# Kernel tuning notes

Hardware: AMD Instinct MI355X
Metric: run time of the kernel (lower is better)

## Reference

```python
import jax, jax.numpy as jnp
import numpy as np

BN_EPS = 1e-3  # Keras BatchNormalization default epsilon

def _conv2d_same(x, w, b):
    # x: NHWC, w: HWIO (kh,kw,2,1)
    y = jax.lax.conv_general_dilated(x, w, window_strides=(1, 1), padding='SAME',
                                     dimension_numbers=('NHWC', 'HWIO', 'NHWC'))
    return y + b

def _zpool(t):
    # concat([max, avg], axis=-1) over channel axis -> last dim = 2
    return jnp.concatenate([jnp.max(t, axis=-1, keepdims=True),
                            jnp.mean(t, axis=-1, keepdims=True)], axis=-1)

def _att_map(t2, w, b, g, beta, mean, var):
    y = _conv2d_same(t2, w, b)
    y = (y - mean) * jax.lax.rsqrt(var + BN_EPS) * g + beta  # inference BN
    return jax.nn.sigmoid(y)

def setup_inputs() -> dict:
    key = jax.random.key(0)
    ks = jax.random.split(key, 8)
    B, H, W, C, K, RR = 32, 56, 56, 256, 7, 8
    d = {}
    d['x'] = jax.random.normal(ks[0], (B, H, W, C), dtype=jnp.float32)
    for i, kk in zip((1, 2, 3), ks[1:4]):
        d[f'conv{i}_w'] = jax.random.normal(kk, (K, K, 2, 1), dtype=jnp.float32) * 0.1
        d[f'conv{i}_b'] = jnp.zeros((1,), dtype=jnp.float32)
        d[f'bn{i}_g'] = jnp.ones((1,), dtype=jnp.float32)
        d[f'bn{i}_b'] = jnp.zeros((1,), dtype=jnp.float32)
        d[f'bn{i}_m'] = jnp.zeros((1,), dtype=jnp.float32)
        d[f'bn{i}_v'] = jnp.ones((1,), dtype=jnp.float32)
    Ch = C // RR
    d['se_w1'] = jax.random.normal(ks[4], (C, Ch), dtype=jnp.float32) * (2.0 / C) ** 0.5
    d['se_b1'] = jnp.zeros((Ch,), dtype=jnp.float32)
    d['se_w2'] = jax.random.normal(ks[5], (Ch, C), dtype=jnp.float32) * 0.05
    d['se_b2'] = jnp.zeros((C,), dtype=jnp.float32)
    return d

def reference(x, conv1_w, conv1_b, bn1_g, bn1_b, bn1_m, bn1_v,
              conv2_w, conv2_b, bn2_g, bn2_b, bn2_m, bn2_v,
              conv3_w, conv3_b, bn3_g, bn3_b, bn3_m, bn3_v,
              se_w1, se_b1, se_w2, se_b2):
    # Branch 1 (H-axis): permute (B,H,W,C)->(B,H,C,W), pool over W
    th1 = jnp.transpose(x, (0, 1, 3, 2))
    a1 = _att_map(_zpool(th1), conv1_w, conv1_b, bn1_g, bn1_b, bn1_m, bn1_v)
    br1 = jnp.transpose(th1 * a1, (0, 1, 3, 2))
    # Branch 2 (W-axis): permute (B,H,W,C)->(B,C,W,H), pool over H
    th2 = jnp.transpose(x, (0, 3, 2, 1))
    a2 = _att_map(_zpool(th2), conv2_w, conv2_b, bn2_g, bn2_b, bn2_m, bn2_v)
    br2 = jnp.transpose(th2 * a2, (0, 3, 2, 1))
    # Branch 3 (identity): pool over C
    a3 = _att_map(_zpool(x), conv3_w, conv3_b, bn3_g, bn3_b, bn3_m, bn3_v)
    br3 = x * a3
    # TriSE1: Add branches, then SE channel gating
    s = br1 + br2 + br3
    gap = jnp.mean(s, axis=(1, 2), keepdims=True)            # (B,1,1,C)
    h = jax.nn.relu(jnp.einsum('bijc,cd->bijd', gap, se_w1) + se_b1)
    cw = jax.nn.sigmoid(jnp.einsum('bijd,dc->bijc', h, se_w2) + se_b2)
    return s * cw
```

## Files before the change

kernel.cpp:

```cpp
#include <hip/hip_runtime.h>
#include <math.h>

namespace {
constexpr int B = 32, H = 56, W = 56, C = 256;
constexpr int HW  = H * W;
constexpr int WC  = W * C;
constexpr int HC  = H * C;
constexpr int HWC = H * W * C;
constexpr int CH  = 32;
constexpr float BN_EPS = 1e-3f;

using f4v = __attribute__((ext_vector_type(4))) float;

__device__ __forceinline__ float sigmoidf_(float v) { return 1.0f / (1.0f + expf(-v)); }

__device__ __forceinline__ void nt_store_float4(float* p, const float4& o) {
    union { float4 s; f4v v; } u;
    u.s = o;
    __builtin_nontemporal_store(u.v, (f4v*)p);
}
}

__global__ __launch_bounds__(256)
void pool_all_kernel(const float* __restrict__ x,
                     float* __restrict__ pmax1, float* __restrict__ pavg1,
                     float* __restrict__ pmax2, float* __restrict__ pavg2,
                     float* __restrict__ pmax3, float* __restrict__ pavg3) {
    const int t = threadIdx.x;
    const int lane = t & 63, sub = t >> 6;
    const int c4 = lane * 4;
    __shared__ float smx[4][256];
    __shared__ float ssm[4][256];

    if (blockIdx.x < B * H) {
        const int b = blockIdx.x / H, h = blockIdx.x % H;
        const float* xp = x + (size_t)b * HWC + (size_t)h * WC + c4;
        float4 v[14];
        #pragma unroll
        for (int wq = 0; wq < 14; ++wq)
            v[wq] = *(const float4*)(xp + (wq * 4 + sub) * C);
        float4 mx = v[0], sm = v[0];
        #pragma unroll
        for (int wq = 1; wq < 14; ++wq) {
            mx.x = fmaxf(mx.x, v[wq].x); mx.y = fmaxf(mx.y, v[wq].y);
            mx.z = fmaxf(mx.z, v[wq].z); mx.w = fmaxf(mx.w, v[wq].w);
            sm.x += v[wq].x; sm.y += v[wq].y; sm.z += v[wq].z; sm.w += v[wq].w;
        }
        #pragma unroll
        for (int wq = 0; wq < 14; ++wq) {
            float m3 = fmaxf(fmaxf(v[wq].x, v[wq].y), fmaxf(v[wq].z, v[wq].w));
            float s3 = v[wq].x + v[wq].y + v[wq].z + v[wq].w;
            #pragma unroll
            for (int off = 32; off > 0; off >>= 1) {
                m3 = fmaxf(m3, __shfl_down(m3, off));
                s3 += __shfl_down(s3, off);
            }
            if (lane == 0) {
                const int w = wq * 4 + sub;
                pmax3[b * HW + h * W + w] = m3;
                pavg3[b * HW + h * W + w] = s3 * (1.0f / C);
            }
        }
        *(float4*)&smx[sub][c4] = mx;
        *(float4*)&ssm[sub][c4] = sm;
        __syncthreads();
        const float m = fmaxf(fmaxf(smx[0][t], smx[1][t]), fmaxf(smx[2][t], smx[3][t]));
        const float s = ssm[0][t] + ssm[1][t] + ssm[2][t] + ssm[3][t];
        pmax1[b * HC + h * C + t] = m;
        pavg1[b * HC + h * C + t] = s * (1.0f / W);
    } else {
        const int tt = blockIdx.x - B * H;
        const int b = tt / W, w = tt % W;
        const float* xp = x + (size_t)b * HWC + (size_t)w * C + c4;
        float4 v[14];
        #pragma unroll
        for (int i = 0; i < 14; ++i)
            v[i] = *(const float4*)(xp + (size_t)(i * 4 + sub) * WC);
        float4 mx = v[0], sm = v[0];
        #pragma unroll
        for (int i = 1; i < 14; ++i) {
            mx.x = fmaxf(mx.x, v[i].x); mx.y = fmaxf(mx.y, v[i].y);
            mx.z = fmaxf(mx.z, v[i].z); mx.w = fmaxf(mx.w, v[i].w);
            sm.x += v[i].x; sm.y += v[i].y; sm.z += v[i].z; sm.w += v[i].w;
        }
        *(float4*)&smx[sub][c4] = mx;
        *(float4*)&ssm[sub][c4] = sm;
        __syncthreads();
        const float m = fmaxf(fmaxf(smx[0][t], smx[1][t]), fmaxf(smx[2][t], smx[3][t]));
        const float s = ssm[0][t] + ssm[1][t] + ssm[2][t] + ssm[3][t];
        pmax2[(size_t)b * WC + w * C + t] = m;
        pavg2[(size_t)b * WC + w * C + t] = s * (1.0f / H);
    }
}

__global__ __launch_bounds__(256)
void conv_all_kernel(const float* __restrict__ pmax1, const float* __restrict__ pavg1,
                     const float* __restrict__ pmax2, const float* __restrict__ pavg2,
                     const float* __restrict__ pmax3, const float* __restrict__ pavg3,
                     const float* __restrict__ c1w, const float* __restrict__ c1b,
                     const float* __restrict__ g1,  const float* __restrict__ be1,
                     const float* __restrict__ m1,  const float* __restrict__ v1,
                     const float* __restrict__ c2w, const float* __restrict__ c2b,
                     const float* __restrict__ g2,  const float* __restrict__ be2,
                     const float* __restrict__ m2,  const float* __restrict__ v2,
                     const float* __restrict__ c3w, const float* __restrict__ c3b,
                     const float* __restrict__ g3,  const float* __restrict__ be3,
                     const float* __restrict__ m3,  const float* __restrict__ v3,
                     float* __restrict__ a1, float* __restrict__ a2t, float* __restrict__ a3) {
    const int t = threadIdx.x;
    __shared__ float wg[98];
    __shared__ float2 sp[7][264];

    if (blockIdx.x < B * H) {
        if (t < 98) wg[t] = c1w[t];
        const int b = blockIdx.x / H, h = blockIdx.x % H;
        const float* bm = pmax1 + (size_t)b * HC;
        const float* ba = pavg1 + (size_t)b * HC;
        #pragma unroll
        for (int ky = 0; ky < 7; ++ky) {
            const int hy = h + ky - 3;
            const bool val = (hy >= 0 && hy < H);
            const int hyc = min(max(hy, 0), H - 1);
            const float lm = bm[hyc * C + t];
            const float la = ba[hyc * C + t];
            sp[ky][t + 3] = val ? make_float2(lm, la) : make_float2(0.f, 0.f);
            if (t < 3) { sp[ky][t] = make_float2(0.f, 0.f); sp[ky][261 - t] = make_float2(0.f, 0.f); }
        }
        __syncthreads();
        const float A  = rsqrtf(v1[0] + BN_EPS) * g1[0];
        const float Bc = (c1b[0] - m1[0]) * A + be1[0];
        float acc = 0.f;
        #pragma unroll
        for (int ky = 0; ky < 7; ++ky)
            #pragma unroll
            for (int kx = 0; kx < 7; ++kx) {
                const float2 p = sp[ky][t + kx];
                acc += p.x * wg[ky * 14 + kx * 2] + p.y * wg[ky * 14 + kx * 2 + 1];
            }
        a1[b * HC + h * C + t] = sigmoidf_(acc * A + Bc);
    } else if (blockIdx.x < 2 * B * H) {
        if (t < 98) wg[t] = c2w[t];
        const int tt = blockIdx.x - B * H;
        const int b = tt / W, w = tt % W;
        #pragma unroll
        for (int kx = 0; kx < 7; ++kx) {
            const int wx = w + kx - 3;
            const bool val = (wx >= 0 && wx < W);
            const int wxc = min(max(wx, 0), W - 1);
            const float lm = pmax2[(size_t)b * WC + wxc * C + t];
            const float la = pavg2[(size_t)b * WC + wxc * C + t];
            sp[kx][t + 3] = val ? make_float2(lm, la) : make_float2(0.f, 0.f);
            if (t < 3) { sp[kx][t] = make_float2(0.f, 0.f); sp[kx][261 - t] = make_float2(0.f, 0.f); }
        }
        __syncthreads();
        const float A  = rsqrtf(v2[0] + BN_EPS) * g2[0];
        const float Bc = (c2b[0] - m2[0]) * A + be2[0];
        float acc = 0.f;
        #pragma unroll
        for (int kx = 0; kx < 7; ++kx)
            #pragma unroll
            for (int ky = 0; ky < 7; ++ky) {
                const float2 p = sp[kx][t + ky];
                acc += p.x * wg[ky * 14 + kx * 2] + p.y * wg[ky * 14 + kx * 2 + 1];
            }
        a2t[(size_t)b * WC + w * C + t] = sigmoidf_(acc * A + Bc);
    } else {
        if (t < 98) wg[t] = c3w[t];
        float2 (*sp3)[66] = (float2(*)[66])sp;
        const int tt = blockIdx.x - 2 * B * H;
        const int b = tt / 14, h0 = (tt % 14) * 4;
        const float* bm = pmax3 + (size_t)b * HW;
        const float* ba = pavg3 + (size_t)b * HW;
        for (int idx = t; idx < 10 * 62; idx += 256) {
            const int r = idx / 62, col = idx % 62;
            const int hh = h0 + r - 3, ww = col - 3;
            const bool val = (hh >= 0 && hh < H && ww >= 0 && ww < W);
            const int hs = min(max(hh, 0), H - 1), wsx = min(max(ww, 0), W - 1);
            const float pm = bm[hs * W + wsx];
            const float pa = ba[hs * W + wsx];
            sp3[r][col] = val ? make_float2(pm, pa) : make_float2(0.f, 0.f);
        }
        __syncthreads();
        if (t < 224) {
            const int r = t / 56, w = t % 56;
            const float A  = rsqrtf(v3[0] + BN_EPS) * g3[0];
            const float Bc = (c3b[0] - m3[0]) * A + be3[0];
            float acc = 0.f;
            #pragma unroll
            for (int ky = 0; ky < 7; ++ky)
                #pragma unroll
                for (int kx = 0; kx < 7; ++kx) {
                    const float2 p = sp3[r + ky][w + kx];
                    acc += p.x * wg[ky * 14 + kx * 2] + p.y * wg[ky * 14 + kx * 2 + 1];
                }
            a3[b * HW + (h0 + r) * W + w] = sigmoidf_(acc * A + Bc);
        }
    }
}

__global__ __launch_bounds__(256)
void gap_row_kernel(const float* __restrict__ x, const float* __restrict__ a3,
                    float* __restrict__ gpart) {
    const int b = blockIdx.x / H, h = blockIdx.x % H;
    const int t = threadIdx.x;
    const int lane = t & 63, sub = t >> 6;
    const int c4 = lane * 4;
    const float* xp = x + (size_t)b * HWC + (size_t)h * WC + c4;
    const float* ap = a3 + b * HW + h * W + sub;
    float4 v[14]; float av[14];
    #pragma unroll
    for (int wq = 0; wq < 14; ++wq) {
        v[wq]  = *(const float4*)(xp + (wq * 4 + sub) * C);
        av[wq] = ap[wq * 4];
    }
    float4 acc = make_float4(0.f, 0.f, 0.f, 0.f);
    #pragma unroll
    for (int wq = 0; wq < 14; ++wq) {
        acc.x += v[wq].x * av[wq];
        acc.y += v[wq].y * av[wq];
        acc.z += v[wq].z * av[wq];
        acc.w += v[wq].w * av[wq];
    }
    __shared__ float sacc[4][256];
    *(float4*)&sacc[sub][c4] = acc;
    __syncthreads();
    gpart[(size_t)blockIdx.x * C + t] = sacc[0][t] + sacc[1][t] + sacc[2][t] + sacc[3][t];
}

__global__ __launch_bounds__(256)
void se_kernel(const float* __restrict__ gpart,
               const float* __restrict__ a1,  const float* __restrict__ pavg1,
               const float* __restrict__ a2t, const float* __restrict__ pavg2,
               const float* __restrict__ w1, const float* __restrict__ b1,
               const float* __restrict__ w2, const float* __restrict__ b2,
               float* __restrict__ cw) {
    const int b = blockIdx.x;
    const int t = threadIdx.x;
    __shared__ float gs[C];
    __shared__ float part[8][33];
    __shared__ float hs[CH];
    const float* pa = a1    + (size_t)b * HC + t;
    const float* pv = pavg1 + (size_t)b * HC + t;
    const float* qa = a2t   + (size_t)b * WC + t;
    const float* qv = pavg2 + (size_t)b * WC + t;
    const float* gp = gpart + (size_t)b * H * C + t;
    float s1 = 0.f, s2 = 0.f, s3 = 0.f;
    #pragma unroll 8
    for (int r = 0; r < H; ++r) {
        s1 += pa[r * C] * pv[r * C];
        s2 += qa[r * C] * qv[r * C];
        s3 += gp[r * C];
    }
    gs[t] = (s1 + s2) * (1.0f / 56.0f) + s3 * (1.0f / (float)HW);
    __syncthreads();
    {
        const int d = t & 31, j = t >> 5;
        float a = 0.f;
        #pragma unroll
        for (int i = 0; i < 32; ++i) {
            const int c = j * 32 + i;
            a += gs[c] * w1[c * CH + d];
        }
        part[j][d] = a;
    }
    __syncthreads();
    if (t < CH) {
        float a = b1[t];
        #pragma unroll
        for (int j = 0; j < 8; ++j) a += part[j][t];
        hs[t] = fmaxf(a, 0.f);
    }
    __syncthreads();
    float a = b2[t];
    #pragma unroll
    for (int d = 0; d < CH; ++d) a += hs[d] * w2[d * C + t];
    cw[b * C + t] = sigmoidf_(a);
}

__global__ __launch_bounds__(256)
void out_row_kernel(const float* __restrict__ x, const float* __restrict__ a1,
                    const float* __restrict__ a2t, const float* __restrict__ a3,
                    const float* __restrict__ cw, float* __restrict__ out) {
    const int b = blockIdx.x / H, h = blockIdx.x % H;
    const int t = threadIdx.x;
    const int lane = t & 63, sub = t >> 6;
    const int c4 = lane * 4;
    const float* xp  = x   + (size_t)b * HWC + (size_t)h * WC + c4;
    const float* a2b = a2t + (size_t)b * WC + c4;
    float*       op  = out + (size_t)b * HWC + (size_t)h * WC + c4;
    const float4 a1v = *(const float4*)(a1 + b * HC + h * C + c4);
    const float4 cwv = *(const float4*)(cw + b * C + c4);
    const float* ap = a3 + b * HW + h * W + sub;
    #pragma unroll
    for (int wq = 0; wq < 14; ++wq) {
        const int off = (wq * 4 + sub) * C;
        const float4 xv  = *(const float4*)(xp  + off);
        const float4 a2v = *(const float4*)(a2b + off);
        const float a3v  = ap[wq * 4];
        float4 o;
        o.x = xv.x * (a1v.x + a2v.x + a3v) * cwv.x;
        o.y = xv.y * (a1v.y + a2v.y + a3v) * cwv.y;
        o.z = xv.z * (a1v.z + a2v.z + a3v) * cwv.z;
        o.w = xv.w * (a1v.w + a2v.w + a3v) * cwv.w;
        nt_store_float4(op + off, o);
    }
}

extern "C" void kernel_launch(void* const* d_in, const int* in_sizes, int n_in,
                              void* d_out, int out_size, void* d_ws, size_t ws_size,
                              hipStream_t stream) {
    const float* x   = (const float*)d_in[0];
    const float* c1w = (const float*)d_in[1];  const float* c1b = (const float*)d_in[2];
    const float* g1  = (const float*)d_in[3];  const float* be1 = (const float*)d_in[4];
    const float* m1  = (const float*)d_in[5];  const float* v1  = (const float*)d_in[6];
    const float* c2w = (const float*)d_in[7];  const float* c2b = (const float*)d_in[8];
    const float* g2  = (const float*)d_in[9];  const float* be2 = (const float*)d_in[10];
    const float* m2  = (const float*)d_in[11]; const float* v2  = (const float*)d_in[12];
    const float* c3w = (const float*)d_in[13]; const float* c3b = (const float*)d_in[14];
    const float* g3  = (const float*)d_in[15]; const float* be3 = (const float*)d_in[16];
    const float* m3  = (const float*)d_in[17]; const float* v3  = (const float*)d_in[18];
    const float* sw1 = (const float*)d_in[19]; const float* sb1 = (const float*)d_in[20];
    const float* sw2 = (const float*)d_in[21]; const float* sb2 = (const float*)d_in[22];

    float* ws = (float*)d_ws;
    float* pmax1 = ws;
    float* pavg1 = pmax1 + (size_t)B * HC;
    float* pmax2 = pavg1 + (size_t)B * HC;
    float* pavg2 = pmax2 + (size_t)B * WC;
    float* pmax3 = pavg2 + (size_t)B * WC;
    float* pavg3 = pmax3 + (size_t)B * HW;
    float* a1    = pavg3 + (size_t)B * HW;
    float* a2t   = a1    + (size_t)B * HC;
    float* a3    = a2t   + (size_t)B * WC;
    float* gpart = a3    + (size_t)B * HW;
    float* cwv   = gpart + (size_t)B * H * C;

    pool_all_kernel<<<B * H + B * W, 256, 0, stream>>>(x, pmax1, pavg1, pmax2, pavg2, pmax3, pavg3);
    conv_all_kernel<<<2 * B * H + B * 14, 256, 0, stream>>>(
        pmax1, pavg1, pmax2, pavg2, pmax3, pavg3,
        c1w, c1b, g1, be1, m1, v1,
        c2w, c2b, g2, be2, m2, v2,
        c3w, c3b, g3, be3, m3, v3,
        a1, a2t, a3);
    gap_row_kernel<<<B * H, 256, 0, stream>>>(x, a3, gpart);
    se_kernel<<<B, 256, 0, stream>>>(gpart, a1, pavg1, a2t, pavg2, sw1, sb1, sw2, sb2, cwv);
    out_row_kernel<<<B * H, 256, 0, stream>>>(x, a1, a2t, a3, cwv, (float*)d_out);
}
```

Measured before the change: 291.4 us.

## Fuse gap row reduction into conv3 blocks and drop nontemporal output stores

```diff
diff --git a/kernel.cpp b/kernel.cpp
--- a/kernel.cpp
+++ b/kernel.cpp
@@ -10,15 +10,7 @@
 constexpr int CH  = 32;
 constexpr float BN_EPS = 1e-3f;
 
-using f4v = __attribute__((ext_vector_type(4))) float;
-
 __device__ __forceinline__ float sigmoidf_(float v) { return 1.0f / (1.0f + expf(-v)); }
-
-__device__ __forceinline__ void nt_store_float4(float* p, const float4& o) {
-    union { float4 s; f4v v; } u;
-    u.s = o;
-    __builtin_nontemporal_store(u.v, (f4v*)p);
-}
 }
 
 __global__ __launch_bounds__(256)
@@ -94,7 +86,8 @@
 }
 
 __global__ __launch_bounds__(256)
-void conv_all_kernel(const float* __restrict__ pmax1, const float* __restrict__ pavg1,
+void conv_all_kernel(const float* __restrict__ x,
+                     const float* __restrict__ pmax1, const float* __restrict__ pavg1,
                      const float* __restrict__ pmax2, const float* __restrict__ pavg2,
                      const float* __restrict__ pmax3, const float* __restrict__ pavg3,
                      const float* __restrict__ c1w, const float* __restrict__ c1b,
@@ -106,68 +99,17 @@
                      const float* __restrict__ c3w, const float* __restrict__ c3b,
                      const float* __restrict__ g3,  const float* __restrict__ be3,
                      const float* __restrict__ m3,  const float* __restrict__ v3,
-                     float* __restrict__ a1, float* __restrict__ a2t, float* __restrict__ a3) {
+                     float* __restrict__ a1, float* __restrict__ a2t, float* __restrict__ a3,
+                     float* __restrict__ gpart) {
     const int t = threadIdx.x;
     __shared__ float wg[98];
     __shared__ float2 sp[7][264];
-
-    if (blockIdx.x < B * H) {
-        if (t < 98) wg[t] = c1w[t];
-        const int b = blockIdx.x / H, h = blockIdx.x % H;
-        const float* bm = pmax1 + (size_t)b * HC;
-        const float* ba = pavg1 + (size_t)b * HC;
-        #pragma unroll
-        for (int ky = 0; ky < 7; ++ky) {
-            const int hy = h + ky - 3;
-            const bool val = (hy >= 0 && hy < H);
-            const int hyc = min(max(hy, 0), H - 1);
-            const float lm = bm[hyc * C + t];
-            const float la = ba[hyc * C + t];
-            sp[ky][t + 3] = val ? make_float2(lm, la) : make_float2(0.f, 0.f);
-            if (t < 3) { sp[ky][t] = make_float2(0.f, 0.f); sp[ky][261 - t] = make_float2(0.f, 0.f); }
-        }
-        __syncthreads();
-        const float A  = rsqrtf(v1[0] + BN_EPS) * g1[0];
-        const float Bc = (c1b[0] - m1[0]) * A + be1[0];
-        float acc = 0.f;
-        #pragma unroll
-        for (int ky = 0; ky < 7; ++ky)
-            #pragma unroll
-            for (int kx = 0; kx < 7; ++kx) {
-                const float2 p = sp[ky][t + kx];
-                acc += p.x * wg[ky * 14 + kx * 2] + p.y * wg[ky * 14 + kx * 2 + 1];
-            }
-        a1[b * HC + h * C + t] = sigmoidf_(acc * A + Bc);
-    } else if (blockIdx.x < 2 * B * H) {
-        if (t < 98) wg[t] = c2w[t];
-        const int tt = blockIdx.x - B * H;
-        const int b = tt / W, w = tt % W;
-        #pragma unroll
-        for (int kx = 0; kx < 7; ++kx) {
-            const int wx = w + kx - 3;
-            const bool val = (wx >= 0 && wx < W);
-            const int wxc = min(max(wx, 0), W - 1);
-            const float lm = pmax2[(size_t)b * WC + wxc * C + t];
-            const float la = pavg2[(size_t)b * WC + wxc * C + t];
-            sp[kx][t + 3] = val ? make_float2(lm, la) : make_float2(0.f, 0.f);
-            if (t < 3) { sp[kx][t] = make_float2(0.f, 0.f); sp[kx][261 - t] = make_float2(0.f, 0.f); }
-        }
-        __syncthreads();
-        const float A  = rsqrtf(v2[0] + BN_EPS) * g2[0];
-        const float Bc = (c2b[0] - m2[0]) * A + be2[0];
-        float acc = 0.f;
-        #pragma unroll
-        for (int kx = 0; kx < 7; ++kx)
-            #pragma unroll
-            for (int ky = 0; ky < 7; ++ky) {
-                const float2 p = sp[kx][t + ky];
-                acc += p.x * wg[ky * 14 + kx * 2] + p.y * wg[ky * 14 + kx * 2 + 1];
-            }
-        a2t[(size_t)b * WC + w * C + t] = sigmoidf_(acc * A + Bc);
-    } else {
+    __shared__ float sa3[4][56];
+
+    if (blockIdx.x < B * 14) {
         if (t < 98) wg[t] = c3w[t];
         float2 (*sp3)[66] = (float2(*)[66])sp;
-        const int tt = blockIdx.x - 2 * B * H;
+        const int tt = blockIdx.x;
         const int b = tt / 14, h0 = (tt % 14) * 4;
         const float* bm = pmax3 + (size_t)b * HW;
         const float* ba = pavg3 + (size_t)b * HW;
@@ -193,38 +135,80 @@
                     const float2 p = sp3[r + ky][w + kx];
                     acc += p.x * wg[ky * 14 + kx * 2] + p.y * wg[ky * 14 + kx * 2 + 1];
                 }
-            a3[b * HW + (h0 + r) * W + w] = sigmoidf_(acc * A + Bc);
-        }
-    }
-}
-
-__global__ __launch_bounds__(256)
-void gap_row_kernel(const float* __restrict__ x, const float* __restrict__ a3,
-                    float* __restrict__ gpart) {
-    const int b = blockIdx.x / H, h = blockIdx.x % H;
-    const int t = threadIdx.x;
-    const int lane = t & 63, sub = t >> 6;
-    const int c4 = lane * 4;
-    const float* xp = x + (size_t)b * HWC + (size_t)h * WC + c4;
-    const float* ap = a3 + b * HW + h * W + sub;
-    float4 v[14]; float av[14];
-    #pragma unroll
-    for (int wq = 0; wq < 14; ++wq) {
-        v[wq]  = *(const float4*)(xp + (wq * 4 + sub) * C);
-        av[wq] = ap[wq * 4];
-    }
-    float4 acc = make_float4(0.f, 0.f, 0.f, 0.f);
-    #pragma unroll
-    for (int wq = 0; wq < 14; ++wq) {
-        acc.x += v[wq].x * av[wq];
-        acc.y += v[wq].y * av[wq];
-        acc.z += v[wq].z * av[wq];
-        acc.w += v[wq].w * av[wq];
-    }
-    __shared__ float sacc[4][256];
-    *(float4*)&sacc[sub][c4] = acc;
-    __syncthreads();
-    gpart[(size_t)blockIdx.x * C + t] = sacc[0][t] + sacc[1][t] + sacc[2][t] + sacc[3][t];
+            const float av = sigmoidf_(acc * A + Bc);
+            a3[b * HW + (h0 + r) * W + w] = av;
+            sa3[r][w] = av;
+        }
+        __syncthreads();
+        const int lane = t & 63, sub = t >> 6;
+        const int c4 = lane * 4;
+        const float* xp = x + (size_t)b * HWC + (size_t)(h0 + sub) * WC + c4;
+        float4 acc4 = make_float4(0.f, 0.f, 0.f, 0.f);
+        #pragma unroll 8
+        for (int w = 0; w < W; ++w) {
+            const float4 xv = *(const float4*)(xp + w * C);
+            const float a3v = sa3[sub][w];
+            acc4.x += xv.x * a3v;
+            acc4.y += xv.y * a3v;
+            acc4.z += xv.z * a3v;
+            acc4.w += xv.w * a3v;
+        }
+        *(float4*)(gpart + (size_t)(b * H + h0 + sub) * C + c4) = acc4;
+    } else if (blockIdx.x < B * 14 + B * H) {
+        if (t < 98) wg[t] = c1w[t];
+        const int tt = blockIdx.x - B * 14;
+        const int b = tt / H, h = tt % H;
+        const float* bm = pmax1 + (size_t)b * HC;
+        const float* ba = pavg1 + (size_t)b * HC;
+        #pragma unroll
+        for (int ky = 0; ky < 7; ++ky) {
+            const int hy = h + ky - 3;
+            const bool val = (hy >= 0 && hy < H);
+            const int hyc = min(max(hy, 0), H - 1);
+            const float lm = bm[hyc * C + t];
+            const float la = ba[hyc * C + t];
+            sp[ky][t + 3] = val ? make_float2(lm, la) : make_float2(0.f, 0.f);
+            if (t < 3) { sp[ky][t] = make_float2(0.f, 0.f); sp[ky][261 - t] = make_float2(0.f, 0.f); }
+        }
+        __syncthreads();
+        const float A  = rsqrtf(v1[0] + BN_EPS) * g1[0];
+        const float Bc = (c1b[0] - m1[0]) * A + be1[0];
+        float acc = 0.f;
+        #pragma unroll
+        for (int ky = 0; ky < 7; ++ky)
+            #pragma unroll
+            for (int kx = 0; kx < 7; ++kx) {
+                const float2 p = sp[ky][t + kx];
+                acc += p.x * wg[ky * 14 + kx * 2] + p.y * wg[ky * 14 + kx * 2 + 1];
+            }
+        a1[b * HC + h * C + t] = sigmoidf_(acc * A + Bc);
+    } else {
+        if (t < 98) wg[t] = c2w[t];
+        const int tt = blockIdx.x - (B * 14 + B * H);
+        const int b = tt / W, w = tt % W;
+        #pragma unroll
+        for (int kx = 0; kx < 7; ++kx) {
+            const int wx = w + kx - 3;
+            const bool val = (wx >= 0 && wx < W);
+            const int wxc = min(max(wx, 0), W - 1);
+            const float lm = pmax2[(size_t)b * WC + wxc * C + t];
+            const float la = pavg2[(size_t)b * WC + wxc * C + t];
+            sp[kx][t + 3] = val ? make_float2(lm, la) : make_float2(0.f, 0.f);
+            if (t < 3) { sp[kx][t] = make_float2(0.f, 0.f); sp[kx][261 - t] = make_float2(0.f, 0.f); }
+        }
+        __syncthreads();
+        const float A  = rsqrtf(v2[0] + BN_EPS) * g2[0];
+        const float Bc = (c2b[0] - m2[0]) * A + be2[0];
+        float acc = 0.f;
+        #pragma unroll
+        for (int kx = 0; kx < 7; ++kx)
+            #pragma unroll
+            for (int ky = 0; ky < 7; ++ky) {
+                const float2 p = sp[kx][t + ky];
+                acc += p.x * wg[ky * 14 + kx * 2] + p.y * wg[ky * 14 + kx * 2 + 1];
+            }
+        a2t[(size_t)b * WC + w * C + t] = sigmoidf_(acc * A + Bc);
+    }
 }
 
 __global__ __launch_bounds__(256)
@@ -302,7 +286,7 @@
         o.y = xv.y * (a1v.y + a2v.y + a3v) * cwv.y;
         o.z = xv.z * (a1v.z + a2v.z + a3v) * cwv.z;
         o.w = xv.w * (a1v.w + a2v.w + a3v) * cwv.w;
-        nt_store_float4(op + off, o);
+        *(float4*)(op + off) = o;
     }
 }
 
@@ -336,13 +320,12 @@
     float* cwv   = gpart + (size_t)B * H * C;
 
     pool_all_kernel<<<B * H + B * W, 256, 0, stream>>>(x, pmax1, pavg1, pmax2, pavg2, pmax3, pavg3);
-    conv_all_kernel<<<2 * B * H + B * 14, 256, 0, stream>>>(
-        pmax1, pavg1, pmax2, pavg2, pmax3, pavg3,
+    conv_all_kernel<<<B * 14 + B * H + B * W, 256, 0, stream>>>(
+        x, pmax1, pavg1, pmax2, pavg2, pmax3, pavg3,
         c1w, c1b, g1, be1, m1, v1,
         c2w, c2b, g2, be2, m2, v2,
         c3w, c3b, g3, be3, m3, v3,
-        a1, a2t, a3);
-    gap_row_kernel<<<B * H, 256, 0, stream>>>(x, a3, gpart);
+        a1, a2t, a3, gpart);
     se_kernel<<<B, 256, 0, stream>>>(gpart, a1, pavg1, a2t, pavg2, sw1, sb1, sw2, sb2, cwv);
     out_row_kernel<<<B * H, 256, 0, stream>>>(x, a1, a2t, a3, cwv, (float*)d_out);
 }
```

Measured after the change: 287.4 us. Within noise of the previous version (-1.4%).
